# Performance work log

Hardware: AMD Instinct MI355X
Metric: run time of the kernel (lower is better)

Reference implementation:

```python
import jax, jax.numpy as jnp
import numpy as np

N, T, F = 20000, 20, 128
H = 128          # lstm hidden per direction
GH, HEADS = 128, 4
NUM_CLASSES = 10
E = 640000
SCALE = 0.05


def _lstm_last_hidden(x, lengths, Wih, Whh, b):
    """Run a unidirectional LSTM over padded x [N,T,F]; return hidden at the
    last valid step per sequence (torch gate order i,f,g,o)."""
    pre = jnp.einsum('ntf,gf->ntg', x, Wih) + b            # [N,T,4H]
    mask = jnp.arange(x.shape[1])[None, :] < lengths[:, None]  # [N,T]
    h0 = jnp.zeros((x.shape[0], Whh.shape[1]), x.dtype)

    def step(carry, inp):
        h, c = carry
        pt, m = inp                                         # [N,4H], [N]
        gates = pt + h @ Whh.T
        i, f, g, o = jnp.split(gates, 4, axis=-1)
        c_new = jax.nn.sigmoid(f) * c + jax.nn.sigmoid(i) * jnp.tanh(g)
        h_new = jax.nn.sigmoid(o) * jnp.tanh(c_new)
        m = m[:, None]
        return (jnp.where(m, h_new, h), jnp.where(m, c_new, c)), None

    (h, _), _ = jax.lax.scan(step, (h0, h0), (pre.transpose(1, 0, 2), mask.T))
    return h


def _reverse_by_length(x, lengths):
    # x[n, t] -> x[n, len-1-t] for t < len (padding positions are masked later)
    idx = jnp.clip(lengths[:, None] - 1 - jnp.arange(x.shape[1])[None, :], 0, None)
    return x[jnp.arange(x.shape[0])[:, None], idx]


def _gat(h, src, dst, W, a_src, a_dst, bias, heads):
    n = h.shape[0]
    xh = (h @ W.T).reshape(n, heads, -1)                    # [N,H,C]
    al_s = jnp.sum(xh * a_src, -1)                          # [N,H]
    al_d = jnp.sum(xh * a_dst, -1)
    e = jax.nn.leaky_relu(al_s[src] + al_d[dst], 0.2)       # [E,H]
    emax = jax.ops.segment_max(e, dst, num_segments=n)
    emax = jnp.where(jnp.isfinite(emax), emax, 0.0)
    ee = jnp.exp(e - emax[dst])
    denom = jax.ops.segment_sum(ee, dst, num_segments=n)
    alpha = ee / (denom[dst] + 1e-16)                       # segment softmax
    out = jax.ops.segment_sum(xh[src] * alpha[..., None], dst, num_segments=n)
    return out.reshape(n, -1) + bias


def setup_inputs() -> dict:
    key = jax.random.key(0)
    ks = jax.random.split(key, 16)
    p = lambda k, *s: jax.random.normal(k, s, jnp.float32) * SCALE
    return {
        'x': jax.random.normal(ks[0], (N, T, F), jnp.float32),
        'lengths': jax.random.randint(ks[1], (N,), 1, T + 1, jnp.int32),
        'edge_index': jax.random.randint(ks[2], (2, E), 0, N, jnp.int32),
        # BiLSTM params (b = b_ih + b_hh combined; identical math)
        'Wih_f': p(ks[3], 4 * H, F), 'Whh_f': p(ks[4], 4 * H, H), 'b_f': p(ks[5], 4 * H),
        'Wih_b': p(ks[6], 4 * H, F), 'Whh_b': p(ks[7], 4 * H, H), 'b_b': p(ks[8], 4 * H),
        # GAT1: in=2H=256 -> heads*GH=512
        'W1': p(ks[9], HEADS * GH, 2 * H), 'a1_src': p(ks[10], HEADS, GH),
        'a1_dst': p(ks[11], HEADS, GH), 'bias1': jnp.zeros((HEADS * GH,), jnp.float32),
        # GAT2: in=512 -> 1*GH=128
        'W2': p(ks[12], GH, HEADS * GH), 'a2_src': p(ks[13], 1, GH),
        'a2_dst': p(ks[14], 1, GH), 'bias2': jnp.zeros((GH,), jnp.float32),
        'Wfc': p(ks[15], NUM_CLASSES, GH), 'bfc': jnp.zeros((NUM_CLASSES,), jnp.float32),
    }


def reference(x, lengths, edge_index, Wih_f, Whh_f, b_f, Wih_b, Whh_b, b_b,
              W1, a1_src, a1_dst, bias1, W2, a2_src, a2_dst, bias2, Wfc, bfc):
    n = x.shape[0]
    h_fwd = _lstm_last_hidden(x, lengths, Wih_f, Whh_f, b_f)
    h_bwd = _lstm_last_hidden(_reverse_by_length(x, lengths), lengths, Wih_b, Whh_b, b_b)
    h = jnp.concatenate([h_fwd, h_bwd], axis=-1)            # [N, 2H]
    # GATConv default adds self-loops
    loop = jnp.arange(n, dtype=edge_index.dtype)
    src = jnp.concatenate([edge_index[0], loop])
    dst = jnp.concatenate([edge_index[1], loop])
    h = jax.nn.relu(_gat(h, src, dst, W1, a1_src, a1_dst, bias1, HEADS))
    h = jax.nn.relu(_gat(h, src, dst, W2, a2_src, a2_dst, bias2, 1))
    return h @ Wfc.T + bfc                                  # [N, num_classes]
```

## Files before the change

kernel.cpp:

```cpp
#include <hip/hip_runtime.h>

#define NSEQ 20000
#define TT 20
#define FD 128
#define EDG 640000
#define ETOT (EDG + NSEQ)

typedef short bf16x8 __attribute__((ext_vector_type(8)));
typedef float f32x4 __attribute__((ext_vector_type(4)));
typedef unsigned short u16;
typedef unsigned int u32;

__device__ __forceinline__ float bf2f(u16 h) {
  union { u32 u; float f; } v; v.u = ((u32)h) << 16; return v.f;
}
__device__ __forceinline__ float bf_lo(u32 w) {
  union { u32 u; float f; } v; v.u = w << 16; return v.f;
}
__device__ __forceinline__ float bf_hi(u32 w) {
  union { u32 u; float f; } v; v.u = w & 0xffff0000u; return v.f;
}
__device__ __forceinline__ u16 f2bf(float f) {
  union { float f; u32 u; } v; v.f = f;
  u32 u = v.u;
  return (u16)((u + 0x7fffu + ((u >> 16) & 1u)) >> 16);
}
__device__ __forceinline__ float fast_rcp(float x) {
  float r; asm("v_rcp_f32 %0, %1" : "=v"(r) : "v"(x)); return r;
}
__device__ __forceinline__ float fast_ex2(float x) {
  float r; asm("v_exp_f32 %0, %1" : "=v"(r) : "v"(x)); return r;
}
__device__ __forceinline__ u32 cvtpk_bf16(float a, float b) {
  u32 r; asm("v_cvt_pk_bf16_f32 %0, %1, %2" : "=v"(r) : "v"(a), "v"(b)); return r;
}
__device__ __forceinline__ int clampi(int v, int lo, int hi) {
  return v < lo ? lo : (v > hi ? hi : v);
}

template<int BF>
__device__ __forceinline__ bf16x8 ld8(const void* p, size_t i) {
  if (BF) return *(const bf16x8*)((const u16*)p + i);
  f32x4 a = *(const f32x4*)((const float*)p + i);
  f32x4 b = *(const f32x4*)((const float*)p + i + 4);
  union { u32 w[4]; bf16x8 v; } u;
  u.w[0] = cvtpk_bf16(a[0], a[1]);
  u.w[1] = cvtpk_bf16(a[2], a[3]);
  u.w[2] = cvtpk_bf16(b[0], b[1]);
  u.w[3] = cvtpk_bf16(b[2], b[3]);
  return u.v;
}

#define OFF_WIHF 0
#define OFF_WHHF 65536
#define OFF_BF   131072
#define OFF_WIHB 131584
#define OFF_WHHB 197120
#define OFF_BB   262656
#define OFF_W1   263168
#define OFF_W2   394240
#define OFF_A1S  459776
#define OFF_A1D  460288
#define OFF_B1   460800
#define OFF_A2S  461312
#define OFF_A2D  461440
#define OFF_B2   461568
#define OFF_WFC  461696
#define OFF_BFC  462976

__global__ void k_detect_zero(const u32* __restrict__ xw, int* __restrict__ flag,
                              int* __restrict__ deg, int* __restrict__ lcnt) {
  int i = blockIdx.x * 256 + threadIdx.x;
  if (i < NSEQ) deg[i] = 0;
  if (i < 64) lcnt[i] = 0;
  if (blockIdx.x == 0 && threadIdx.x < 64) {
    u16 lo = (u16)(xw[threadIdx.x] & 0xffffu);
    int e = (lo >> 7) & 0xff;
    unsigned long long m = __ballot(e >= 100 && e <= 140);
    if (threadIdx.x == 0) flag[0] = (__popcll(m) >= 32) ? 1 : 0;
  }
}

struct CvtArgs {
  const void* src[16];
  int off[16];
  int cnt[16];
  int wt[16];
};

template<int BF>
__global__ void k_cvt(CvtArgs a, u16* __restrict__ canon, const int* __restrict__ flag) {
  if (flag[0] != BF) return;
  int idx = blockIdx.x * 256 + threadIdx.x;
  int stride = gridDim.x * 256;
#pragma unroll 1
  for (int s = 0; s < 16; ++s) {
    const void* sp = a.src[s];
    int n = a.cnt[s], off = a.off[s], wt = a.wt[s];
    for (int i = idx; i < n; i += stride) {
      float v = BF ? bf2f(((const u16*)sp)[i]) : ((const float*)sp)[i];
      if (wt) {
        int gate = (wt == 1) ? ((i >> 14) & 3) : ((i >> 7) & 3);
        v *= (gate == 2) ? 2.885390082f : -1.442695041f;
      }
      canon[off + i] = f2bf(v);
    }
  }
}

__global__ void k_fill0(u16* __restrict__ out, int n) {
  int i = blockIdx.x * 256 + threadIdx.x;
  if (i < n) out[i] = 0;
}

template<int BF>
__global__ __launch_bounds__(512, 2) void k_lstm(
    const void* __restrict__ x, const int* __restrict__ lengths,
    const int* __restrict__ lperm,
    const u16* __restrict__ canon, u16* __restrict__ hcat,
    const int* __restrict__ flag)
{
  if (flag[0] != BF) return;
  __shared__ u16 Ax[2][128 * 128];
  __shared__ u16 Ah[2][128 * 128];
  __shared__ int lenS[128];
  __shared__ int seqS[128];

  const int tid = threadIdx.x;
  const int wv = tid >> 6;
  const int lane = tid & 63;
  const int q = lane >> 4;
  const int cc = lane & 15;
  const int dir = blockIdx.y;
  const int b0 = (gridDim.x - 1 - blockIdx.x) * 128;

  const u16* Wi = canon + (dir ? OFF_WIHB : OFF_WIHF);
  const u16* Wh = canon + (dir ? OFF_WHHB : OFF_WHHF);
  const u16* bb = canon + (dir ? OFF_BB : OFF_BF);

  bf16x8 wih[4][4], whh[4][4];
  uint2 bvp[4];
#pragma unroll
  for (int g = 0; g < 4; ++g) {
    int row = g * 128 + wv * 16 + cc;
#pragma unroll
    for (int kt = 0; kt < 4; ++kt) {
      wih[g][kt] = *(const bf16x8*)(Wi + row * 128 + kt * 32 + q * 8);
      whh[g][kt] = *(const bf16x8*)(Wh + row * 128 + kt * 32 + q * 8);
    }
    bvp[g] = *(const uint2*)(bb + g * 128 + wv * 16 + q * 4);
  }

  if (tid < 128) {
    int s = lperm[clampi(b0 + tid, 0, NSEQ - 1)];
    s = clampi(s, 0, NSEQ - 1);
    seqS[tid] = s;
    lenS[tid] = clampi(lengths[s], 1, TT);
  }
  {
    f32x4 zz = {0.f, 0.f, 0.f, 0.f};
    f32x4* p = (f32x4*)Ah[0];
    for (int i = tid; i < 2048; i += 512) p[i] = zz;
  }
  __syncthreads();

  const int tmax = lenS[127];

  int lenq[8];
#pragma unroll
  for (int m = 0; m < 8; ++m) lenq[m] = lenS[m * 16 + cc];

  int axj[4], lenj[4];
  size_t xbj[4];
#pragma unroll
  for (int j = 0; j < 4; ++j) {
    int idx = tid + j * 512;
    int row = idx >> 4, ch = idx & 15;
    axj[j] = row * 128 + ((ch ^ (row & 15)) * 8);
    xbj[j] = (size_t)seqS[row] * (TT * FD) + ch * 8;
    lenj[j] = lenS[row];
  }

  int rofs[4];
#pragma unroll
  for (int kt = 0; kt < 4; ++kt) rofs[kt] = cc * 128 + (((4 * kt + q) ^ cc) * 8);
  const int awbase = cc * 128 + (((wv * 2 + (q >> 1)) ^ cc) * 8) + (q & 1) * 4;

  {
#pragma unroll
    for (int j = 0; j < 4; ++j) {
      int t0 = dir ? (lenj[j] - 1) : 0;
      bf16x8 d = ld8<BF>(x, xbj[j] + t0 * FD);
      *(bf16x8*)&Ax[0][axj[j]] = d;
    }
  }
  float c[8][4] = {};
  int cb = 0;
  __syncthreads();

#pragma unroll 1
  for (int t = 0; t < tmax; ++t) {
    const u16* Axr = Ax[cb];
    u16* Axw = Ax[cb ^ 1];
    const u16* Ahr = Ah[cb];
    u16* Ahw = Ah[cb ^ 1];

    bf16x8 d[4];
    const bool more = (t + 1 < tmax);
    if (more) {
#pragma unroll
      for (int j = 0; j < 4; ++j) {
        int tt2 = dir ? (lenj[j] - 1 - (t + 1)) : (t + 1);
        if (tt2 < 0) tt2 = 0;
        d[j] = ld8<BF>(x, xbj[j] + tt2 * FD);
      }
    }

#pragma unroll
    for (int m = 0; m < 8; ++m) {
      const int mb = m * 2048;
      f32x4 acc[4];
#pragma unroll
      for (int g = 0; g < 4; ++g) {
        f32x4 vi = {bf_lo(bvp[g].x), bf_hi(bvp[g].x), bf_lo(bvp[g].y), bf_hi(bvp[g].y)};
        acc[g] = vi;
      }
#pragma unroll
      for (int kt = 0; kt < 4; ++kt) {
        bf16x8 b = *(const bf16x8*)&Axr[mb + rofs[kt]];
#pragma unroll
        for (int g = 0; g < 4; ++g)
          acc[g] = __builtin_amdgcn_mfma_f32_16x16x32_bf16(wih[g][kt], b, acc[g], 0, 0, 0);
      }
#pragma unroll
      for (int kt = 0; kt < 4; ++kt) {
        bf16x8 b = *(const bf16x8*)&Ahr[mb + rofs[kt]];
#pragma unroll
        for (int g = 0; g < 4; ++g)
          acc[g] = __builtin_amdgcn_mfma_f32_16x16x32_bf16(whh[g][kt], b, acc[g], 0, 0, 0);
      }

      uint2 hw;
      if (t < lenq[m]) {
        float hf[4];
#pragma unroll
        for (int r = 0; r < 4; ++r) {
          float Ei = fast_ex2(acc[0][r]);
          float Ef = fast_ex2(acc[1][r]);
          float G  = fast_ex2(acc[2][r]) + 1.0f;
          float Eo = fast_ex2(acc[3][r]);
          float A = 1.0f + Ef, B = 1.0f + Ei;
          float BG = B * G;
          float num = c[m][r] * BG + (A * G - 2.0f * A);
          float cn = num * fast_rcp(A * BG);
          c[m][r] = cn;
          float C2 = fast_ex2(cn * 2.885390082f) + 1.0f;
          hf[r] = (C2 - 2.0f) * fast_rcp((1.0f + Eo) * C2);
        }
        hw.x = cvtpk_bf16(hf[0], hf[1]);
        hw.y = cvtpk_bf16(hf[2], hf[3]);
      } else {
        hw = *(const uint2*)&Ahr[mb + awbase];
      }
      *(uint2*)&Ahw[mb + awbase] = hw;
    }

    if (more) {
#pragma unroll
      for (int j = 0; j < 4; ++j) *(bf16x8*)&Axw[axj[j]] = d[j];
    }
    __syncthreads();
    cb ^= 1;
  }

  for (int i = tid; i < 2048; i += 512) {
    int row = i >> 4, ch = i & 15;
    if (b0 + row < NSEQ) {
      int seq = seqS[row];
      bf16x8 v = *(const bf16x8*)&Ah[cb][row * 128 + ((ch ^ (row & 15)) * 8)];
      *(bf16x8*)(hcat + (size_t)seq * 256 + dir * 128 + ch * 8) = v;
    }
  }
}

__global__ __launch_bounds__(256) void k_gemm(
    const u16* __restrict__ A, const u16* __restrict__ W, u16* __restrict__ C,
    int M, int Nc, int K,
    const u16* __restrict__ aS, const u16* __restrict__ aD,
    float* __restrict__ als, float* __restrict__ ald, int alsStride)
{
  __shared__ u16 As[128 * 64];
  __shared__ u16 Bs[128 * 64];
  const int tid = threadIdx.x;
  const int wv = tid >> 6, lane = tid & 63, q = lane >> 4, cc = lane & 15;
  const int mblk = blockIdx.x * 128, nblk = blockIdx.y * 128;
  const int wm = (wv & 1) * 64, wn = (wv >> 1) * 64;

  f32x4 acc[4][4] = {};

  const int srow = tid >> 1;
  const int sc0 = (tid & 1) * 4;
  int arow_g = mblk + srow; if (arow_g > M - 1) arow_g = M - 1;
  const u16* aptr = A + (size_t)arow_g * K + sc0 * 8;
  const u16* bptr = W + (size_t)(nblk + srow) * K + sc0 * 8;

  for (int k0 = 0; k0 < K; k0 += 64) {
#pragma unroll
    for (int cch = 0; cch < 4; ++cch) {
      bf16x8 av = *(const bf16x8*)(aptr + k0 + cch * 8);
      bf16x8 bvv = *(const bf16x8*)(bptr + k0 + cch * 8);
      int ch = sc0 + cch;
      *(bf16x8*)&As[srow * 64 + ((ch ^ (srow & 7)) * 8)] = av;
      *(bf16x8*)&Bs[srow * 64 + ((ch ^ (srow & 7)) * 8)] = bvv;
    }
    __syncthreads();
#pragma unroll
    for (int kt = 0; kt < 2; ++kt) {
      bf16x8 af[4];
#pragma unroll
      for (int m = 0; m < 4; ++m) {
        int row = wm + m * 16 + cc;
        af[m] = *(const bf16x8*)&As[row * 64 + (((4 * kt + q) ^ (row & 7)) * 8)];
      }
#pragma unroll
      for (int n = 0; n < 4; ++n) {
        int rowb = wn + n * 16 + cc;
        bf16x8 bfr = *(const bf16x8*)&Bs[rowb * 64 + (((4 * kt + q) ^ (rowb & 7)) * 8)];
#pragma unroll
        for (int m = 0; m < 4; ++m)
          acc[m][n] = __builtin_amdgcn_mfma_f32_16x16x32_bf16(bfr, af[m], acc[m][n], 0, 0, 0);
      }
    }
    __syncthreads();
  }

  float pls[4] = {}, pld[4] = {};
#pragma unroll
  for (int n = 0; n < 4; ++n) {
    uint2 ws = *(const uint2*)(aS + nblk + wn + n * 16 + q * 4);
    uint2 wd = *(const uint2*)(aD + nblk + wn + n * 16 + q * 4);
    float s0 = bf_lo(ws.x), s1 = bf_hi(ws.x), s2 = bf_lo(ws.y), s3 = bf_hi(ws.y);
    float d0 = bf_lo(wd.x), d1 = bf_hi(wd.x), d2 = bf_lo(wd.y), d3 = bf_hi(wd.y);
#pragma unroll
    for (int m = 0; m < 4; ++m) {
      int row = mblk + wm + m * 16 + cc;
      uint2 st;
      st.x = cvtpk_bf16(acc[m][n][0], acc[m][n][1]);
      st.y = cvtpk_bf16(acc[m][n][2], acc[m][n][3]);
      if (row < M) *(uint2*)(C + (size_t)row * Nc + nblk + wn + n * 16 + q * 4) = st;
      pls[m] += acc[m][n][0] * s0 + acc[m][n][1] * s1 + acc[m][n][2] * s2 + acc[m][n][3] * s3;
      pld[m] += acc[m][n][0] * d0 + acc[m][n][1] * d1 + acc[m][n][2] * d2 + acc[m][n][3] * d3;
    }
  }

#pragma unroll
  for (int m = 0; m < 4; ++m) {
    pls[m] += __shfl_xor(pls[m], 16, 64);
    pls[m] += __shfl_xor(pls[m], 32, 64);
    pld[m] += __shfl_xor(pld[m], 16, 64);
    pld[m] += __shfl_xor(pld[m], 32, 64);
  }
  float* sred = (float*)As;
  if (lane < 16) {
#pragma unroll
    for (int m = 0; m < 4; ++m) {
      int idx = ((wv & 1) * 4 + m) * 32 + cc * 2 + (wv >> 1);
      sred[idx] = pls[m];
      sred[256 + idx] = pld[m];
    }
  }
  __syncthreads();
  if (wv < 2) {
    int m = lane >> 4, ccc = lane & 15;
    int row = mblk + wv * 64 + m * 16 + ccc;
    int idx = (wv * 4 + m) * 32 + ccc * 2;
    if (row < M) {
      als[(size_t)row * alsStride + blockIdx.y] = sred[idx] + sred[idx + 1];
      ald[(size_t)row * alsStride + blockIdx.y] = sred[256 + idx] + sred[256 + idx + 1];
    }
  }
}

__global__ __launch_bounds__(256) void k_agg1(
    const u16* __restrict__ xh1, const float* __restrict__ als, const float* __restrict__ ald,
    const int* __restrict__ offs, const int* __restrict__ csr,
    const u16* __restrict__ canon, u16* __restrict__ h1)
{
  const int lane = threadIdx.x & 63;
  const int n = blockIdx.x * 4 + (threadIdx.x >> 6);
  int off0 = offs[n], off1 = offs[n + 1];
  off0 = clampi(off0, 0, ETOT);
  off1 = clampi(off1, off0, ETOT);
  const int deg = off1 - off0;
  const float4 ad = *(const float4*)(ald + (size_t)n * 4);
  const u16* xb = xh1 + lane * 2;

  float o0 = 0.f, o1 = 0.f, o2 = 0.f, o3 = 0.f, o4 = 0.f, o5 = 0.f, o6 = 0.f, o7 = 0.f;
  if (deg <= 64) {
    int s = 0;
    float e0 = -1e30f, e1 = -1e30f, e2 = -1e30f, e3 = -1e30f;
    if (lane < deg) {
      s = clampi(csr[off0 + lane], 0, NSEQ - 1);
      float4 av = *(const float4*)(als + (size_t)s * 4);
      float t;
      t = av.x + ad.x; e0 = t > 0.f ? t : 0.2f * t;
      t = av.y + ad.y; e1 = t > 0.f ? t : 0.2f * t;
      t = av.z + ad.z; e2 = t > 0.f ? t : 0.2f * t;
      t = av.w + ad.w; e3 = t > 0.f ? t : 0.2f * t;
    }
    float m0 = e0, m1 = e1, m2 = e2, m3 = e3;
#pragma unroll
    for (int off = 32; off >= 1; off >>= 1) {
      m0 = fmaxf(m0, __shfl_xor(m0, off, 64));
      m1 = fmaxf(m1, __shfl_xor(m1, off, 64));
      m2 = fmaxf(m2, __shfl_xor(m2, off, 64));
      m3 = fmaxf(m3, __shfl_xor(m3, off, 64));
    }
    float x0 = (lane < deg) ? __expf(e0 - m0) : 0.f;
    float x1 = (lane < deg) ? __expf(e1 - m1) : 0.f;
    float x2 = (lane < deg) ? __expf(e2 - m2) : 0.f;
    float x3 = (lane < deg) ? __expf(e3 - m3) : 0.f;
    float s0 = x0, s1 = x1, s2 = x2, s3 = x3;
#pragma unroll
    for (int off = 32; off >= 1; off >>= 1) {
      s0 += __shfl_xor(s0, off, 64);
      s1 += __shfl_xor(s1, off, 64);
      s2 += __shfl_xor(s2, off, 64);
      s3 += __shfl_xor(s3, off, 64);
    }
    float a0 = x0 * fast_rcp(s0 + 1e-16f);
    float a1 = x1 * fast_rcp(s1 + 1e-16f);
    float a2 = x2 * fast_rcp(s2 + 1e-16f);
    float a3 = x3 * fast_rcp(s3 + 1e-16f);
    const int sofs = s * 512;
#pragma unroll 2
    for (int j = 0; j < deg; ++j) {
      int so = __builtin_amdgcn_readlane(sofs, j);
      float aa0 = __int_as_float(__builtin_amdgcn_readlane(__float_as_int(a0), j));
      float aa1 = __int_as_float(__builtin_amdgcn_readlane(__float_as_int(a1), j));
      float aa2 = __int_as_float(__builtin_amdgcn_readlane(__float_as_int(a2), j));
      float aa3 = __int_as_float(__builtin_amdgcn_readlane(__float_as_int(a3), j));
      u32 v0 = *(const u32*)(xb + so);
      u32 v1 = *(const u32*)(xb + so + 128);
      u32 v2 = *(const u32*)(xb + so + 256);
      u32 v3 = *(const u32*)(xb + so + 384);
      o0 += aa0 * bf_lo(v0); o1 += aa0 * bf_hi(v0);
      o2 += aa1 * bf_lo(v1); o3 += aa1 * bf_hi(v1);
      o4 += aa2 * bf_lo(v2); o5 += aa2 * bf_hi(v2);
      o6 += aa3 * bf_lo(v3); o7 += aa3 * bf_hi(v3);
    }
  } else {
    float m0 = -1e30f, m1 = -1e30f, m2 = -1e30f, m3 = -1e30f;
    for (int k = off0 + lane; k < off1; k += 64) {
      int s = clampi(csr[k], 0, NSEQ - 1);
      float4 av = *(const float4*)(als + (size_t)s * 4);
      float t;
      t = av.x + ad.x; t = t > 0.f ? t : 0.2f * t; m0 = fmaxf(m0, t);
      t = av.y + ad.y; t = t > 0.f ? t : 0.2f * t; m1 = fmaxf(m1, t);
      t = av.z + ad.z; t = t > 0.f ? t : 0.2f * t; m2 = fmaxf(m2, t);
      t = av.w + ad.w; t = t > 0.f ? t : 0.2f * t; m3 = fmaxf(m3, t);
    }
#pragma unroll
    for (int off = 32; off >= 1; off >>= 1) {
      m0 = fmaxf(m0, __shfl_xor(m0, off, 64));
      m1 = fmaxf(m1, __shfl_xor(m1, off, 64));
      m2 = fmaxf(m2, __shfl_xor(m2, off, 64));
      m3 = fmaxf(m3, __shfl_xor(m3, off, 64));
    }
    float s0 = 0.f, s1 = 0.f, s2 = 0.f, s3 = 0.f;
    for (int k = off0 + lane; k < off1; k += 64) {
      int s = clampi(csr[k], 0, NSEQ - 1);
      float4 av = *(const float4*)(als + (size_t)s * 4);
      float t;
      t = av.x + ad.x; t = t > 0.f ? t : 0.2f * t; s0 += __expf(t - m0);
      t = av.y + ad.y; t = t > 0.f ? t : 0.2f * t; s1 += __expf(t - m1);
      t = av.z + ad.z; t = t > 0.f ? t : 0.2f * t; s2 += __expf(t - m2);
      t = av.w + ad.w; t = t > 0.f ? t : 0.2f * t; s3 += __expf(t - m3);
    }
#pragma unroll
    for (int off = 32; off >= 1; off >>= 1) {
      s0 += __shfl_xor(s0, off, 64);
      s1 += __shfl_xor(s1, off, 64);
      s2 += __shfl_xor(s2, off, 64);
      s3 += __shfl_xor(s3, off, 64);
    }
    float rd0 = fast_rcp(s0 + 1e-16f), rd1 = fast_rcp(s1 + 1e-16f);
    float rd2 = fast_rcp(s2 + 1e-16f), rd3 = fast_rcp(s3 + 1e-16f);
    for (int k = off0; k < off1; ++k) {
      int s = clampi(csr[k], 0, NSEQ - 1);
      float4 av = *(const float4*)(als + (size_t)s * 4);
      float t;
      t = av.x + ad.x; t = t > 0.f ? t : 0.2f * t; float aa0 = __expf(t - m0) * rd0;
      t = av.y + ad.y; t = t > 0.f ? t : 0.2f * t; float aa1 = __expf(t - m1) * rd1;
      t = av.z + ad.z; t = t > 0.f ? t : 0.2f * t; float aa2 = __expf(t - m2) * rd2;
      t = av.w + ad.w; t = t > 0.f ? t : 0.2f * t; float aa3 = __expf(t - m3) * rd3;
      const u16* xr = xb + (size_t)s * 512;
      u32 v0 = *(const u32*)(xr);
      u32 v1 = *(const u32*)(xr + 128);
      u32 v2 = *(const u32*)(xr + 256);
      u32 v3 = *(const u32*)(xr + 384);
      o0 += aa0 * bf_lo(v0); o1 += aa0 * bf_hi(v0);
      o2 += aa1 * bf_lo(v1); o3 += aa1 * bf_hi(v1);
      o4 += aa2 * bf_lo(v2); o5 += aa2 * bf_hi(v2);
      o6 += aa3 * bf_lo(v3); o7 += aa3 * bf_hi(v3);
    }
  }
  float b0 = bf2f(canon[OFF_B1 + lane * 2]),       b1 = bf2f(canon[OFF_B1 + lane * 2 + 1]);
  float b2 = bf2f(canon[OFF_B1 + 128 + lane * 2]), b3 = bf2f(canon[OFF_B1 + 128 + lane * 2 + 1]);
  float b4 = bf2f(canon[OFF_B1 + 256 + lane * 2]), b5 = bf2f(canon[OFF_B1 + 256 + lane * 2 + 1]);
  float b6 = bf2f(canon[OFF_B1 + 384 + lane * 2]), b7 = bf2f(canon[OFF_B1 + 384 + lane * 2 + 1]);
  o0 += b0; o1 += b1; o2 += b2; o3 += b3; o4 += b4; o5 += b5; o6 += b6; o7 += b7;
  o0 = o0 > 0.f ? o0 : 0.f; o1 = o1 > 0.f ? o1 : 0.f;
  o2 = o2 > 0.f ? o2 : 0.f; o3 = o3 > 0.f ? o3 : 0.f;
  o4 = o4 > 0.f ? o4 : 0.f; o5 = o5 > 0.f ? o5 : 0.f;
  o6 = o6 > 0.f ? o6 : 0.f; o7 = o7 > 0.f ? o7 : 0.f;
  u16* hb = h1 + (size_t)n * 512 + lane * 2;
  *(u32*)(hb)       = cvtpk_bf16(o0, o1);
  *(u32*)(hb + 128) = cvtpk_bf16(o2, o3);
  *(u32*)(hb + 256) = cvtpk_bf16(o4, o5);
  *(u32*)(hb + 384) = cvtpk_bf16(o6, o7);
}

__global__ __launch_bounds__(256) void k_agg2(
    const u16* __restrict__ xh2, const float* __restrict__ als2, const float* __restrict__ ald2,
    const int* __restrict__ offs, const int* __restrict__ csr,
    const u16* __restrict__ canon, void* __restrict__ out, const int* __restrict__ flag)
{
  const int lane = threadIdx.x & 63;
  const int n = blockIdx.x * 4 + (threadIdx.x >> 6);
  int off0 = offs[n], off1 = offs[n + 1];
  off0 = clampi(off0, 0, ETOT);
  off1 = clampi(off1, off0, ETOT);
  const float adn = ald2[n];
  const int deg = off1 - off0;

  float o0 = 0.f, o1 = 0.f;
  if (deg <= 64) {
    int s = 0;
    float e = -1e30f;
    if (lane < deg) {
      s = clampi(csr[off0 + lane], 0, NSEQ - 1);
      float t = als2[s] + adn;
      e = t > 0.f ? t : 0.2f * t;
    }
    float mx = e;
#pragma unroll
    for (int off = 32; off >= 1; off >>= 1) mx = fmaxf(mx, __shfl_xor(mx, off, 64));
    float ex = (lane < deg) ? __expf(e - mx) : 0.f;
    float sm = ex;
#pragma unroll
    for (int off = 32; off >= 1; off >>= 1) sm += __shfl_xor(sm, off, 64);
    const float a = ex * fast_rcp(sm + 1e-16f);
    const int sofs = s * 128;
#pragma unroll 4
    for (int j = 0; j < deg; ++j) {
      int so = __builtin_amdgcn_readlane(sofs, j);
      float aa = __int_as_float(__builtin_amdgcn_readlane(__float_as_int(a), j));
      u32 xv = *(const u32*)(xh2 + so + lane * 2);
      o0 += aa * bf_lo(xv);
      o1 += aa * bf_hi(xv);
    }
  } else {
    float mx = -1e30f;
    for (int k = off0 + lane; k < off1; k += 64) {
      float e = als2[clampi(csr[k], 0, NSEQ - 1)] + adn;
      e = e > 0.f ? e : 0.2f * e;
      mx = fmaxf(mx, e);
    }
#pragma unroll
    for (int off = 32; off >= 1; off >>= 1) mx = fmaxf(mx, __shfl_xor(mx, off, 64));
    float sm = 0.f;
    for (int k = off0 + lane; k < off1; k += 64) {
      float e = als2[clampi(csr[k], 0, NSEQ - 1)] + adn;
      e = e > 0.f ? e : 0.2f * e;
      sm += __expf(e - mx);
    }
#pragma unroll
    for (int off = 32; off >= 1; off >>= 1) sm += __shfl_xor(sm, off, 64);
    float rd = fast_rcp(sm + 1e-16f);
#pragma unroll 4
    for (int k = off0; k < off1; ++k) {
      int s = clampi(csr[k], 0, NSEQ - 1);
      float e = als2[s] + adn;
      e = e > 0.f ? e : 0.2f * e;
      float a = __expf(e - mx) * rd;
      u32 xv = *(const u32*)(xh2 + (size_t)s * 128 + lane * 2);
      o0 += a * bf_lo(xv);
      o1 += a * bf_hi(xv);
    }
  }
  o0 += bf2f(canon[OFF_B2 + lane * 2]);     o0 = o0 > 0.f ? o0 : 0.f;
  o1 += bf2f(canon[OFF_B2 + lane * 2 + 1]); o1 = o1 > 0.f ? o1 : 0.f;

  float res[10];
#pragma unroll
  for (int cls = 0; cls < 10; ++cls) {
    float p = o0 * bf2f(canon[OFF_WFC + cls * 128 + lane * 2]) +
              o1 * bf2f(canon[OFF_WFC + cls * 128 + lane * 2 + 1]);
#pragma unroll
    for (int off = 32; off >= 1; off >>= 1) p += __shfl_xor(p, off, 64);
    float v = p + bf2f(canon[OFF_BFC + cls]);
    res[cls] = (fabsf(v) < 1e30f) ? v : 0.f;
  }
  if (flag[0]) {
    if (lane < 5) {
      u32 pk = (u32)f2bf(res[lane * 2]) | ((u32)f2bf(res[lane * 2 + 1]) << 16);
      ((u32*)out)[(size_t)n * 5 + lane] = pk;
    }
  } else {
    if (lane < 10) ((float*)out)[(size_t)n * 10 + lane] = res[lane];
  }
}

__global__ void k_hist_all(const int* __restrict__ ei, const int* __restrict__ lengths,
                           int* __restrict__ deg, int* __restrict__ lcnt) {
  int i = blockIdx.x * 256 + threadIdx.x;
  if (i < ETOT) {
    int d = (i < EDG) ? ei[EDG + i] : (i - EDG);
    d = clampi(d, 0, NSEQ - 1);
    atomicAdd(&deg[d], 1);
  }
  if (i < NSEQ) atomicAdd(&lcnt[clampi(lengths[i], 1, TT) - 1], 1);
}

__global__ __launch_bounds__(1024) void k_scan(const int* __restrict__ deg,
                                               int* __restrict__ offs, int* __restrict__ cur,
                                               const int* __restrict__ lcnt,
                                               int* __restrict__ lcur) {
  __shared__ int wsum[16];
  const int tid = threadIdx.x;
  if (tid == 0) {
    int run = 0;
    for (int i = 0; i < TT; ++i) { lcur[i] = run; run += lcnt[i]; }
  }
  const int lane = tid & 63, wv = tid >> 6;
  const int CHUNK = 20;
  int base = tid * CHUNK;
  int loc[20];
  int s = 0;
#pragma unroll
  for (int i = 0; i < CHUNK; ++i) {
    int idx = base + i;
    int v = (idx < NSEQ) ? deg[idx] : 0;
    loc[i] = s;
    s += v;
  }
  int inc = s;
#pragma unroll
  for (int off = 1; off < 64; off <<= 1) {
    int t2 = __shfl_up(inc, off, 64);
    if (lane >= off) inc += t2;
  }
  if (lane == 63) wsum[wv] = inc;
  __syncthreads();
  int wbase = 0;
  for (int i = 0; i < wv; ++i) wbase += wsum[i];
  int tbase = wbase + inc - s;
#pragma unroll
  for (int i = 0; i < CHUNK; ++i) {
    int idx = base + i;
    if (idx < NSEQ) {
      int st = tbase + loc[i];
      offs[idx] = st;
      cur[idx] = st;
    }
  }
  if (tid == 0) offs[NSEQ] = ETOT;
}

__global__ void k_scatter_all(const int* __restrict__ ei, const int* __restrict__ lengths,
                              int* __restrict__ cur, int* __restrict__ csr,
                              int* __restrict__ lcur, int* __restrict__ lperm) {
  int i = blockIdx.x * 256 + threadIdx.x;
  if (i < ETOT) {
    int s, d;
    if (i < EDG) { s = ei[i]; d = ei[EDG + i]; }
    else { s = i - EDG; d = s; }
    d = clampi(d, 0, NSEQ - 1);
    int pos = atomicAdd(&cur[d], 1);
    pos = clampi(pos, 0, ETOT - 1);
    csr[pos] = s;
  }
  if (i < NSEQ) {
    int b = clampi(lengths[i], 1, TT) - 1;
    int pos = atomicAdd(&lcur[b], 1);
    lperm[clampi(pos, 0, NSEQ - 1)] = i;
  }
}

extern "C" void kernel_launch(void* const* d_in, const int* in_sizes, int n_in,
                              void* d_out, int out_size, void* d_ws, size_t ws_size,
                              hipStream_t stream) {
  (void)in_sizes; (void)n_in;
  const void* x     = d_in[0];
  const int* lengths= (const int*)d_in[1];
  const int* ei     = (const int*)d_in[2];

  const size_t NEED = 45769344u;
  if (ws_size < NEED) {
    k_fill0<<<(out_size + 255) / 256, 256, 0, stream>>>((u16*)d_out, out_size);
    return;
  }

  char* w = (char*)d_ws;
  size_t o = 0;
  auto alloc = [&](size_t b) { char* p = w + o; o += (b + 255) & ~(size_t)255; return p; };
  int*  flag = (int*)  alloc(256);
  u16*  canon= (u16*)  alloc(1048576);
  int*  deg  = (int*)  alloc((size_t)NSEQ * 4);
  int*  offs = (int*)  alloc((size_t)(NSEQ + 1) * 4);
  int*  cur  = (int*)  alloc((size_t)NSEQ * 4);
  int*  csr  = (int*)  alloc((size_t)ETOT * 4);
  float* als1= (float*)alloc((size_t)NSEQ * 4 * 4);
  float* ald1= (float*)alloc((size_t)NSEQ * 4 * 4);
  char* regB = alloc((size_t)NSEQ * 512 * 2);
  u16*  xh1  = (u16*)regB;
  u16*  xh2  = (u16*)regB;
  float* als2= (float*)(regB + (size_t)NSEQ * 128 * 2 + (size_t)NSEQ * 128 * 4);
  float* ald2= als2 + NSEQ;
  char* regA = alloc((size_t)NSEQ * 256 * 2);
  u16*  hcat = (u16*)regA;
  u16*  h1   = (u16*)regA;
  alloc((size_t)NSEQ * 256 * 2);

  int* lperm = (int*)regB;
  int* lcnt  = (int*)(regB + 80128);
  int* lcur  = (int*)(regB + 80256);

  k_detect_zero<<<(NSEQ + 255) / 256, 256, 0, stream>>>((const u32*)x, flag, deg, lcnt);

  CvtArgs ca;
  const int srcIdx[16] = {3, 4, 5, 6, 7, 8, 9, 13, 10, 11, 12, 14, 15, 16, 17, 18};
  const int offv[16]   = {OFF_WIHF, OFF_WHHF, OFF_BF, OFF_WIHB, OFF_WHHB, OFF_BB,
                          OFF_W1, OFF_W2, OFF_A1S, OFF_A1D, OFF_B1,
                          OFF_A2S, OFF_A2D, OFF_B2, OFF_WFC, OFF_BFC};
  const int cntv[16]   = {65536, 65536, 512, 65536, 65536, 512,
                          131072, 65536, 512, 512, 512, 128, 128, 128, 1280, 10};
  const int wtv[16]    = {1, 1, 2, 1, 1, 2, 0, 0, 0, 0, 0, 0, 0, 0, 0, 0};
  for (int i = 0; i < 16; ++i) {
    ca.src[i] = d_in[srcIdx[i]]; ca.off[i] = offv[i]; ca.cnt[i] = cntv[i]; ca.wt[i] = wtv[i];
  }
  k_cvt<1><<<256, 256, 0, stream>>>(ca, canon, flag);
  k_cvt<0><<<256, 256, 0, stream>>>(ca, canon, flag);

  k_hist_all<<<(ETOT + 255) / 256, 256, 0, stream>>>(ei, lengths, deg, lcnt);
  k_scan<<<1, 1024, 0, stream>>>(deg, offs, cur, lcnt, lcur);
  k_scatter_all<<<(ETOT + 255) / 256, 256, 0, stream>>>(ei, lengths, cur, csr, lcur, lperm);

  k_lstm<1><<<dim3(157, 2), 512, 0, stream>>>(x, lengths, lperm, canon, hcat, flag);
  k_lstm<0><<<dim3(157, 2), 512, 0, stream>>>(x, lengths, lperm, canon, hcat, flag);

  k_gemm<<<dim3(157, 4), 256, 0, stream>>>(hcat, canon + OFF_W1, xh1, NSEQ, 512, 256,
                                           canon + OFF_A1S, canon + OFF_A1D, als1, ald1, 4);
  k_agg1<<<5000, 256, 0, stream>>>(xh1, als1, ald1, offs, csr, canon, h1);

  k_gemm<<<dim3(157, 1), 256, 0, stream>>>(h1, canon + OFF_W2, xh2, NSEQ, 128, 512,
                                           canon + OFF_A2S, canon + OFF_A2D, als2, ald2, 1);
  k_agg2<<<5000, 256, 0, stream>>>(xh2, als2, ald2, offs, csr, canon, d_out, flag);
}
```

Measured before the change: 801.0 us.

## Halve LSTM tile to 64 sequences per block and swap grid axes

Each LSTM block now handles 64 length-sorted sequences instead of 128, so 626 blocks are launched instead of 314 and shared memory per block is halved. The grid is reordered so the direction is the fast-varying axis, which co-schedules the forward and backward blocks of the same sequence tile. Smaller tiles follow the sorted lengths more closely, so fewer blocks run up to a long tmax, and more blocks fill the CUs. The cost is that each block reloads the same weights into registers for half as much work. Separately, the unroll factor of the GAT layer-1 aggregation loop goes from 2 to 4.

```diff
diff --git a/kernel.cpp b/kernel.cpp
--- a/kernel.cpp
+++ b/kernel.cpp
@@ -121,18 +121,18 @@
     const int* __restrict__ flag)
 {
   if (flag[0] != BF) return;
-  __shared__ u16 Ax[2][128 * 128];
-  __shared__ u16 Ah[2][128 * 128];
-  __shared__ int lenS[128];
-  __shared__ int seqS[128];
+  __shared__ u16 Ax[2][64 * 128];
+  __shared__ u16 Ah[2][64 * 128];
+  __shared__ int lenS[64];
+  __shared__ int seqS[64];
 
   const int tid = threadIdx.x;
   const int wv = tid >> 6;
   const int lane = tid & 63;
   const int q = lane >> 4;
   const int cc = lane & 15;
-  const int dir = blockIdx.y;
-  const int b0 = (gridDim.x - 1 - blockIdx.x) * 128;
+  const int dir = blockIdx.x;
+  const int b0 = (gridDim.y - 1 - blockIdx.y) * 64;
 
   const u16* Wi = canon + (dir ? OFF_WIHB : OFF_WIHF);
   const u16* Wh = canon + (dir ? OFF_WHHB : OFF_WHHF);
@@ -151,7 +151,7 @@
     bvp[g] = *(const uint2*)(bb + g * 128 + wv * 16 + q * 4);
   }
 
-  if (tid < 128) {
+  if (tid < 64) {
     int s = lperm[clampi(b0 + tid, 0, NSEQ - 1)];
     s = clampi(s, 0, NSEQ - 1);
     seqS[tid] = s;
@@ -160,26 +160,23 @@
   {
     f32x4 zz = {0.f, 0.f, 0.f, 0.f};
     f32x4* p = (f32x4*)Ah[0];
-    for (int i = tid; i < 2048; i += 512) p[i] = zz;
+    for (int i = tid; i < 1024; i += 512) p[i] = zz;
   }
   __syncthreads();
 
-  const int tmax = lenS[127];
-
-  int lenq[8];
-#pragma unroll
-  for (int m = 0; m < 8; ++m) lenq[m] = lenS[m * 16 + cc];
-
-  int axj[4], lenj[4];
-  size_t xbj[4];
-#pragma unroll
-  for (int j = 0; j < 4; ++j) {
-    int idx = tid + j * 512;
-    int row = idx >> 4, ch = idx & 15;
-    axj[j] = row * 128 + ((ch ^ (row & 15)) * 8);
-    xbj[j] = (size_t)seqS[row] * (TT * FD) + ch * 8;
-    lenj[j] = lenS[row];
-  }
+  const int tmax = lenS[63];
+
+  int lenq[4];
+#pragma unroll
+  for (int m = 0; m < 4; ++m) lenq[m] = lenS[m * 16 + cc];
+
+  const int lrow = tid >> 3;
+  const int lj = tid & 7;
+  const int sL = seqS[lrow];
+  const int lenL = lenS[lrow];
+  const size_t xbase = (size_t)sL * (TT * FD);
+  const int ax0 = lrow * 128 + ((lj ^ (lrow & 15)) * 8);
+  const int ax1 = lrow * 128 + (((lj + 8) ^ (lrow & 15)) * 8);
 
   int rofs[4];
 #pragma unroll
@@ -187,14 +184,13 @@
   const int awbase = cc * 128 + (((wv * 2 + (q >> 1)) ^ cc) * 8) + (q & 1) * 4;
 
   {
-#pragma unroll
-    for (int j = 0; j < 4; ++j) {
-      int t0 = dir ? (lenj[j] - 1) : 0;
-      bf16x8 d = ld8<BF>(x, xbj[j] + t0 * FD);
-      *(bf16x8*)&Ax[0][axj[j]] = d;
-    }
-  }
-  float c[8][4] = {};
+    int t0 = dir ? (lenL - 1) : 0;
+    bf16x8 d0 = ld8<BF>(x, xbase + t0 * FD + lj * 8);
+    bf16x8 d1 = ld8<BF>(x, xbase + t0 * FD + (lj + 8) * 8);
+    *(bf16x8*)&Ax[0][ax0] = d0;
+    *(bf16x8*)&Ax[0][ax1] = d1;
+  }
+  float c[4][4] = {};
   int cb = 0;
   __syncthreads();
 
@@ -205,19 +201,18 @@
     const u16* Ahr = Ah[cb];
     u16* Ahw = Ah[cb ^ 1];
 
-    bf16x8 d[4];
+    bf16x8 d0 = {}, d1 = {};
     const bool more = (t + 1 < tmax);
     if (more) {
-#pragma unroll
-      for (int j = 0; j < 4; ++j) {
-        int tt2 = dir ? (lenj[j] - 1 - (t + 1)) : (t + 1);
-        if (tt2 < 0) tt2 = 0;
-        d[j] = ld8<BF>(x, xbj[j] + tt2 * FD);
-      }
-    }
-
-#pragma unroll
-    for (int m = 0; m < 8; ++m) {
+      int tn = t + 1;
+      int tt2 = dir ? (lenL - 1 - tn) : tn;
+      if (tt2 < 0) tt2 = 0;
+      d0 = ld8<BF>(x, xbase + tt2 * FD + lj * 8);
+      d1 = ld8<BF>(x, xbase + tt2 * FD + (lj + 8) * 8);
+    }
+
+#pragma unroll
+    for (int m = 0; m < 4; ++m) {
       const int mb = m * 2048;
       f32x4 acc[4];
 #pragma unroll
@@ -266,14 +261,14 @@
     }
 
     if (more) {
-#pragma unroll
-      for (int j = 0; j < 4; ++j) *(bf16x8*)&Axw[axj[j]] = d[j];
+      *(bf16x8*)&Axw[ax0] = d0;
+      *(bf16x8*)&Axw[ax1] = d1;
     }
     __syncthreads();
     cb ^= 1;
   }
 
-  for (int i = tid; i < 2048; i += 512) {
+  for (int i = tid; i < 1024; i += 512) {
     int row = i >> 4, ch = i & 15;
     if (b0 + row < NSEQ) {
       int seq = seqS[row];
@@ -433,7 +428,7 @@
     float a2 = x2 * fast_rcp(s2 + 1e-16f);
     float a3 = x3 * fast_rcp(s3 + 1e-16f);
     const int sofs = s * 512;
-#pragma unroll 2
+#pragma unroll 4
     for (int j = 0; j < deg; ++j) {
       int so = __builtin_amdgcn_readlane(sofs, j);
       float aa0 = __int_as_float(__builtin_amdgcn_readlane(__float_as_int(a0), j));
@@ -747,8 +742,8 @@
   k_scan<<<1, 1024, 0, stream>>>(deg, offs, cur, lcnt, lcur);
   k_scatter_all<<<(ETOT + 255) / 256, 256, 0, stream>>>(ei, lengths, cur, csr, lcur, lperm);
 
-  k_lstm<1><<<dim3(157, 2), 512, 0, stream>>>(x, lengths, lperm, canon, hcat, flag);
-  k_lstm<0><<<dim3(157, 2), 512, 0, stream>>>(x, lengths, lperm, canon, hcat, flag);
+  k_lstm<1><<<dim3(2, 313), 512, 0, stream>>>(x, lengths, lperm, canon, hcat, flag);
+  k_lstm<0><<<dim3(2, 313), 512, 0, stream>>>(x, lengths, lperm, canon, hcat, flag);
 
   k_gemm<<<dim3(157, 4), 256, 0, stream>>>(hcat, canon + OFF_W1, xh1, NSEQ, 512, 256,
                                            canon + OFF_A1S, canon + OFF_A1D, als1, ald1, 4);
```

After: 748.1 us. 6.6% less time.
